# Performance work log

Hardware: AMD Instinct MI355X
Metric: run time of the kernel (lower is better)

The kernel has to match this reference:

```python
import jax, jax.numpy as jnp
import numpy as np

B, S, D, H = 2, 2048, 1024, 16
HD = D // H  # head dim = 64


def setup_inputs() -> dict:
    key = jax.random.key(0)
    ks = jax.random.split(key, 11)
    s = 0.02
    return {
        "query": jax.random.normal(ks[0], (B, S, D), jnp.float32),
        "key": jax.random.normal(ks[1], (B, S, D), jnp.float32),
        "value": jax.random.normal(ks[2], (B, S, D), jnp.float32),
        "Wq": jax.random.normal(ks[3], (D, D), jnp.float32) * s,
        "bq": jnp.zeros((D,), jnp.float32),
        "Wk": jax.random.normal(ks[4], (D, D), jnp.float32) * s,
        "bk": jnp.zeros((D,), jnp.float32),
        "Wv": jax.random.normal(ks[5], (D, D), jnp.float32) * s,
        "bv": jnp.zeros((D,), jnp.float32),
        "Wo": jax.random.normal(ks[6], (D, D), jnp.float32) * s,
        "bo": jnp.zeros((D,), jnp.float32),
    }


def reference(query, key, value, Wq, bq, Wk, bk, Wv, bv, Wo, bo):
    # Linear projections (torch Linear: x @ W^T + b; here W stored as [in, out])
    q = query @ Wq + bq  # [B,S,D]
    k = key @ Wk + bk
    v = value @ Wv + bv
    # split heads -> [B,H,S,HD]
    q = q.reshape(B, S, H, HD).transpose(0, 2, 1, 3)
    k = k.reshape(B, S, H, HD).transpose(0, 2, 1, 3)
    v = v.reshape(B, S, H, HD).transpose(0, 2, 1, 3)
    scores = jnp.einsum("bhqd,bhkd->bhqk", q, k) / jnp.sqrt(jnp.float32(HD))
    probs = jax.nn.softmax(scores, axis=-1)
    # dropout is identity at inference
    ctx = jnp.einsum("bhqk,bhkd->bhqd", probs, v)
    ctx = ctx.transpose(0, 2, 1, 3).reshape(B, S, D)
    return ctx @ Wo + bo
```

## Files before the change

kernel.cpp:

```cpp
#include <hip/hip_runtime.h>

#define BB 2
#define SS 2048
#define DD 1024
#define HH 16
#define HD 64
#define MM (BB*SS)

typedef __attribute__((ext_vector_type(8))) short bf16x8;
typedef __attribute__((ext_vector_type(4))) float f32x4;

static __device__ inline unsigned short f2bf(float x) {
    unsigned int u = __float_as_uint(x);
    unsigned int r = (u + 0x7fffu + ((u >> 16) & 1u)) >> 16;
    return (unsigned short)r;
}

static __device__ inline unsigned pack2bf(float lo, float hi) {
    return (unsigned)f2bf(lo) | ((unsigned)f2bf(hi) << 16);
}

static __device__ inline f32x4 mfma16(bf16x8 a, bf16x8 b, f32x4 c) {
    return __builtin_amdgcn_mfma_f32_16x16x32_bf16(a, b, c, 0, 0, 0);
}

static __device__ inline float fast_exp2(float x) {
    return __builtin_amdgcn_exp2f(x);
}

typedef __attribute__((address_space(3))) unsigned int lds_u32;
typedef const __attribute__((address_space(1))) unsigned int glb_u32;
static __device__ inline void async_ld16(const void* g, void* l) {
    __builtin_amdgcn_global_load_lds((glb_u32*)g, (lds_u32*)l, 16, 0, 0);
}

__global__ __launch_bounds__(256) void convert3_f32_bf16(const float* __restrict__ a,
                                                         const float* __restrict__ b,
                                                         const float* __restrict__ c,
                                                         unsigned short* __restrict__ oa,
                                                         unsigned short* __restrict__ ob,
                                                         unsigned short* __restrict__ oc,
                                                         int n) {
    const float* in = (blockIdx.z == 0) ? a : (blockIdx.z == 1) ? b : c;
    unsigned short* out = (blockIdx.z == 0) ? oa : (blockIdx.z == 1) ? ob : oc;
    int i = (blockIdx.x * 256 + threadIdx.x) * 4;
    if (i + 3 < n) {
        float4 v = *(const float4*)(in + i);
        ushort4 o;
        o.x = f2bf(v.x); o.y = f2bf(v.y); o.z = f2bf(v.z); o.w = f2bf(v.w);
        *(ushort4*)(out + i) = o;
    }
}

struct W4Args {
    const float* src[4];
    unsigned short* dst[4];
};
__global__ __launch_bounds__(256) void transpose4_f32_bf16(W4Args args) {
    __shared__ float tile[32][33];
    const float* in = args.src[blockIdx.z];
    unsigned short* out = args.dst[blockIdx.z];
    int c0 = blockIdx.x * 32, r0 = blockIdx.y * 32;
    int x = threadIdx.x;
    for (int yy = threadIdx.y; yy < 32; yy += 8)
        tile[yy][x] = in[(size_t)(r0 + yy) * DD + c0 + x];
    __syncthreads();
    for (int yy = threadIdx.y; yy < 32; yy += 8)
        out[(size_t)(c0 + yy) * DD + r0 + x] = f2bf(tile[x][yy]);
}

__global__ __launch_bounds__(256) void transpose_bf16_batched(const unsigned short* __restrict__ in,
                                                              unsigned short* __restrict__ out,
                                                              int R, int C) {
    __shared__ unsigned short tile[32][33];
    int z = blockIdx.z;
    const unsigned short* ib = in + (size_t)z * R * C;
    unsigned short* ob = out + (size_t)z * R * C;
    int c0 = blockIdx.x * 32, r0 = blockIdx.y * 32;
    int x = threadIdx.x;
    for (int yy = threadIdx.y; yy < 32; yy += 8)
        tile[yy][x] = ib[(size_t)(r0 + yy) * C + c0 + x];
    __syncthreads();
    for (int yy = threadIdx.y; yy < 32; yy += 8)
        ob[(size_t)(c0 + yy) * R + r0 + x] = tile[x][yy];
}

__device__ inline void cstore(float* C, size_t idx, float v) { C[idx] = v; }
__device__ inline void cstore(unsigned short* C, size_t idx, float v) { C[idx] = f2bf(v); }

template <typename OutT>
__device__ inline void gemm_bt_body(const unsigned short* __restrict__ A,
                                    const unsigned short* __restrict__ Bt,
                                    const float* __restrict__ bias,
                                    OutT* __restrict__ C,
                                    int M, int N, int K, float scale) {
    __shared__ alignas(16) unsigned short As[128 * 32];
    __shared__ alignas(16) unsigned short Bs[128 * 32];
    const int t = threadIdx.x;
    const int lane = t & 63, wave = t >> 6;
    const int quad = lane >> 4, l15 = lane & 15;
    const int wm = wave & 1, wn = wave >> 1;
    const int m0 = blockIdx.y * 128, n0 = blockIdx.x * 128;

    const unsigned short* gA = A + (size_t)(m0 + wave * 32 + (lane >> 2)) * K + (lane & 3) * 8;
    const unsigned short* gB = Bt + (size_t)(n0 + wave * 32 + (lane >> 2)) * K + (lane & 3) * 8;
    unsigned short* lA0 = &As[(wave * 32) * 32];
    unsigned short* lA1 = &As[(wave * 32 + 16) * 32];
    unsigned short* lB0 = &Bs[(wave * 32) * 32];
    unsigned short* lB1 = &Bs[(wave * 32 + 16) * 32];

    f32x4 acc[4][4];
#pragma unroll
    for (int i = 0; i < 4; i++)
#pragma unroll
        for (int j = 0; j < 4; j++) acc[i][j] = (f32x4){0.f, 0.f, 0.f, 0.f};

    for (int k0 = 0; k0 < K; k0 += 32) {
        __syncthreads();
        async_ld16(gA + k0, lA0);
        async_ld16(gA + (size_t)16 * K + k0, lA1);
        async_ld16(gB + k0, lB0);
        async_ld16(gB + (size_t)16 * K + k0, lB1);
        __syncthreads();

        bf16x8 af[4], bfr[4];
#pragma unroll
        for (int i = 0; i < 4; i++)
            af[i] = *(const bf16x8*)&As[(wm * 64 + i * 16 + l15) * 32 + quad * 8];
#pragma unroll
        for (int j = 0; j < 4; j++)
            bfr[j] = *(const bf16x8*)&Bs[(wn * 64 + j * 16 + l15) * 32 + quad * 8];
#pragma unroll
        for (int i = 0; i < 4; i++)
#pragma unroll
            for (int j = 0; j < 4; j++)
                acc[i][j] = mfma16(af[i], bfr[j], acc[i][j]);
    }

#pragma unroll
    for (int j = 0; j < 4; j++) {
        int col = n0 + wn * 64 + j * 16 + l15;
        float bv = bias[col];
#pragma unroll
        for (int i = 0; i < 4; i++) {
            int rowb = m0 + wm * 64 + i * 16 + quad * 4;
#pragma unroll
            for (int rr = 0; rr < 4; rr++) {
                float v = (acc[i][j][rr] + bv) * scale;
                cstore(C, (size_t)(rowb + rr) * N + col, v);
            }
        }
    }
}

struct QKVArgs {
    const unsigned short* A[3];
    const unsigned short* Bt[3];
    const float* bias[3];
    unsigned short* C[3];
};

#define QSCALE 0.1803368801111204f

__global__ __launch_bounds__(256) void gemm_qkv(QKVArgs args) {
    int z = blockIdx.z;
    float scale = (z == 0) ? QSCALE : 1.0f;
    gemm_bt_body<unsigned short>(args.A[z], args.Bt[z], args.bias[z], args.C[z],
                                 MM, DD, DD, scale);
}

__global__ __launch_bounds__(256) void gemm_out(const unsigned short* __restrict__ A,
                                                const unsigned short* __restrict__ Bt,
                                                const float* __restrict__ bias,
                                                float* __restrict__ C) {
    gemm_bt_body<float>(A, Bt, bias, C, MM, DD, DD, 1.0f);
}

#define TK 64
#define NTILE (SS / TK)
#define LDP 72

static __device__ inline void kv_step_lds(const unsigned short* __restrict__ Ksb,
                                          const unsigned short* __restrict__ Vsb,
                                          int kb0, bf16x8 qa0, bf16x8 qa1,
                                          f32x4 (&o)[4], float& lrow,
                                          int quad, int l15) {
    bf16x8 k0 = *(const bf16x8*)&Ksb[(kb0 + l15) * LDP + quad * 8];
    bf16x8 k1 = *(const bf16x8*)&Ksb[(kb0 + l15) * LDP + 32 + quad * 8];
    bf16x8 k2 = *(const bf16x8*)&Ksb[(kb0 + 16 + l15) * LDP + quad * 8];
    bf16x8 k3 = *(const bf16x8*)&Ksb[(kb0 + 16 + l15) * LDP + 32 + quad * 8];

    f32x4 sc0 = (f32x4){0.f, 0.f, 0.f, 0.f};
    f32x4 sc1 = (f32x4){0.f, 0.f, 0.f, 0.f};
    sc0 = mfma16(k0, qa0, sc0);
    sc0 = mfma16(k1, qa1, sc0);
    sc1 = mfma16(k2, qa0, sc1);
    sc1 = mfma16(k3, qa1, sc1);

    float p[8];
#pragma unroll
    for (int rr = 0; rr < 4; rr++) {
        p[rr]     = fast_exp2(sc0[rr]);
        p[rr + 4] = fast_exp2(sc1[rr]);
    }
    lrow += (p[0] + p[1]) + (p[2] + p[3]) + (p[4] + p[5]) + (p[6] + p[7]);

    union { unsigned u[4]; bf16x8 v; } pf;
    pf.u[0] = pack2bf(p[0], p[1]);
    pf.u[1] = pack2bf(p[2], p[3]);
    pf.u[2] = pack2bf(p[4], p[5]);
    pf.u[3] = pack2bf(p[6], p[7]);

#pragma unroll
    for (int j = 0; j < 4; j++) {
        union { ushort4 s[2]; bf16x8 v; } af;
        af.s[0] = *(const ushort4*)&Vsb[(j * 16 + l15) * LDP + kb0 + quad * 4];
        af.s[1] = *(const ushort4*)&Vsb[(j * 16 + l15) * LDP + kb0 + 16 + quad * 4];
        o[j] = mfma16(af.v, pf.v, o[j]);
    }
}

__global__ __launch_bounds__(256, 4) void flash_attn(const unsigned short* __restrict__ Q,
                                                     const unsigned short* __restrict__ Kg,
                                                     const unsigned short* __restrict__ Vt,
                                                     unsigned short* __restrict__ ctx) {
    __shared__ alignas(16) unsigned short Ks[2][TK * LDP];
    __shared__ alignas(16) unsigned short Vs[2][TK * LDP];
    const int t = threadIdx.x;
    const int lane = t & 63, wave = t >> 6;
    const int quad = lane >> 4, l15 = lane & 15;
    const int qg = blockIdx.x & 31;
    const int bh = blockIdx.x >> 5;
    const int h = bh & 15, b = bh >> 4;
    const int q0 = (qg * 4 + wave) * 16;

    const unsigned short* Qb = Q + (size_t)b * SS * DD + h * HD;
    const unsigned short* Kb = Kg + (size_t)b * SS * DD + h * HD;
    const unsigned short* Vb = Vt + ((size_t)b * DD + h * HD) * SS;

    const int r0 = t >> 3, cs = t & 7;
    const unsigned short* gK = Kb + (size_t)r0 * DD + cs * 8;
    const unsigned short* gV = Vb + (size_t)r0 * SS + cs * 8;
    const int ldsoff0 = r0 * LDP + cs * 8;
    const int ldsoff1 = (r0 + 32) * LDP + cs * 8;

    bf16x8 qa0 = *(const bf16x8*)(Qb + (size_t)(q0 + l15) * DD + quad * 8);
    bf16x8 qa1 = *(const bf16x8*)(Qb + (size_t)(q0 + l15) * DD + 32 + quad * 8);

    float lrow = 0.f;
    f32x4 o[4];
#pragma unroll
    for (int j = 0; j < 4; j++) o[j] = (f32x4){0.f, 0.f, 0.f, 0.f};

    {
        uint4 kr0 = *(const uint4*)(gK);
        uint4 kr1 = *(const uint4*)(gK + (size_t)32 * DD);
        uint4 vr0 = *(const uint4*)(gV);
        uint4 vr1 = *(const uint4*)(gV + (size_t)32 * SS);
        *(uint4*)&Ks[0][ldsoff0] = kr0;
        *(uint4*)&Ks[0][ldsoff1] = kr1;
        *(uint4*)&Vs[0][ldsoff0] = vr0;
        *(uint4*)&Vs[0][ldsoff1] = vr1;
    }
    __syncthreads();

    for (int tile = 0; tile < NTILE; ++tile) {
        const int buf = tile & 1;
        uint4 kr0, kr1, vr0, vr1;
        if (tile + 1 < NTILE) {
            const unsigned short* gKn = gK + (size_t)(tile + 1) * TK * DD;
            const unsigned short* gVn = gV + (tile + 1) * TK;
            kr0 = *(const uint4*)(gKn);
            kr1 = *(const uint4*)(gKn + (size_t)32 * DD);
            vr0 = *(const uint4*)(gVn);
            vr1 = *(const uint4*)(gVn + (size_t)32 * SS);
        }
        kv_step_lds(Ks[buf], Vs[buf], 0, qa0, qa1, o, lrow, quad, l15);
        kv_step_lds(Ks[buf], Vs[buf], 32, qa0, qa1, o, lrow, quad, l15);
        if (tile + 1 < NTILE) {
            __syncthreads();
            *(uint4*)&Ks[buf ^ 1][ldsoff0] = kr0;
            *(uint4*)&Ks[buf ^ 1][ldsoff1] = kr1;
            *(uint4*)&Vs[buf ^ 1][ldsoff0] = vr0;
            *(uint4*)&Vs[buf ^ 1][ldsoff1] = vr1;
            __syncthreads();
        }
    }

    lrow += __shfl_xor(lrow, 16, 64);
    lrow += __shfl_xor(lrow, 32, 64);
    float linv = 1.0f / lrow;

    unsigned short* crow = ctx + ((size_t)b * SS + q0 + l15) * DD + h * HD;
#pragma unroll
    for (int j = 0; j < 4; j++) {
        ushort4 w;
        w.x = f2bf(o[j][0] * linv); w.y = f2bf(o[j][1] * linv);
        w.z = f2bf(o[j][2] * linv); w.w = f2bf(o[j][3] * linv);
        *(ushort4*)(crow + j * 16 + quad * 4) = w;
    }
}

extern "C" void kernel_launch(void* const* d_in, const int* in_sizes, int n_in,
                              void* d_out, int out_size, void* d_ws, size_t ws_size,
                              hipStream_t stream) {
    const float* query = (const float*)d_in[0];
    const float* key   = (const float*)d_in[1];
    const float* value = (const float*)d_in[2];
    const float* Wq = (const float*)d_in[3];
    const float* bq = (const float*)d_in[4];
    const float* Wk = (const float*)d_in[5];
    const float* bk = (const float*)d_in[6];
    const float* Wv = (const float*)d_in[7];
    const float* bv = (const float*)d_in[8];
    const float* Wo = (const float*)d_in[9];
    const float* bo = (const float*)d_in[10];
    float* out = (float*)d_out;

    char* ws = (char*)d_ws;
    const size_t WSZ = (size_t)DD * DD * 2;
    const size_t XSZ = (size_t)MM * DD * 2;
    unsigned short* Wqt = (unsigned short*)(ws + 0 * WSZ);
    unsigned short* Wkt = (unsigned short*)(ws + 1 * WSZ);
    unsigned short* Wvt = (unsigned short*)(ws + 2 * WSZ);
    unsigned short* Wot = (unsigned short*)(ws + 3 * WSZ);
    unsigned short* Xq  = (unsigned short*)(ws + 4 * WSZ);
    unsigned short* Xk  = (unsigned short*)(ws + 4 * WSZ + 1 * XSZ);
    unsigned short* Xv  = (unsigned short*)(ws + 4 * WSZ + 2 * XSZ);
    unsigned short* Qp  = (unsigned short*)(ws + 4 * WSZ + 3 * XSZ);
    unsigned short* Kp  = (unsigned short*)(ws + 4 * WSZ + 4 * XSZ);
    unsigned short* Vp  = (unsigned short*)(ws + 4 * WSZ + 5 * XSZ);
    unsigned short* Vtp = Xq;
    unsigned short* ctx = Xk;

    const int n_act = MM * DD;

    convert3_f32_bf16<<<dim3(n_act / (256 * 4), 1, 3), 256, 0, stream>>>(
        query, key, value, Xq, Xk, Xv, n_act);

    W4Args wargs;
    wargs.src[0] = Wq; wargs.src[1] = Wk; wargs.src[2] = Wv; wargs.src[3] = Wo;
    wargs.dst[0] = Wqt; wargs.dst[1] = Wkt; wargs.dst[2] = Wvt; wargs.dst[3] = Wot;
    transpose4_f32_bf16<<<dim3(DD / 32, DD / 32, 4), dim3(32, 8), 0, stream>>>(wargs);

    QKVArgs args;
    args.A[0] = Xq; args.A[1] = Xk; args.A[2] = Xv;
    args.Bt[0] = Wqt; args.Bt[1] = Wkt; args.Bt[2] = Wvt;
    args.bias[0] = bq; args.bias[1] = bk; args.bias[2] = bv;
    args.C[0] = Qp; args.C[1] = Kp; args.C[2] = Vp;
    gemm_qkv<<<dim3(DD / 128, MM / 128, 3), 256, 0, stream>>>(args);

    transpose_bf16_batched<<<dim3(DD / 32, SS / 32, BB), dim3(32, 8), 0, stream>>>(Vp, Vtp, SS, DD);

    flash_attn<<<BB * HH * 32, 256, 0, stream>>>(Qp, Kp, Vtp, ctx);

    gemm_out<<<dim3(DD / 128, MM / 128), 256, 0, stream>>>(ctx, Wot, bo, out);
}
```

Measured before the change: 255.0 us.

## Merge prep kernels, fuse V transpose into QKV GEMM, double query rows per wave

```diff
diff --git a/kernel.cpp b/kernel.cpp
--- a/kernel.cpp
+++ b/kernel.cpp
@@ -34,55 +34,39 @@
     __builtin_amdgcn_global_load_lds((glb_u32*)g, (lds_u32*)l, 16, 0, 0);
 }
 
-__global__ __launch_bounds__(256) void convert3_f32_bf16(const float* __restrict__ a,
-                                                         const float* __restrict__ b,
-                                                         const float* __restrict__ c,
-                                                         unsigned short* __restrict__ oa,
-                                                         unsigned short* __restrict__ ob,
-                                                         unsigned short* __restrict__ oc,
-                                                         int n) {
-    const float* in = (blockIdx.z == 0) ? a : (blockIdx.z == 1) ? b : c;
-    unsigned short* out = (blockIdx.z == 0) ? oa : (blockIdx.z == 1) ? ob : oc;
-    int i = (blockIdx.x * 256 + threadIdx.x) * 4;
-    if (i + 3 < n) {
-        float4 v = *(const float4*)(in + i);
-        ushort4 o;
-        o.x = f2bf(v.x); o.y = f2bf(v.y); o.z = f2bf(v.z); o.w = f2bf(v.w);
-        *(ushort4*)(out + i) = o;
-    }
-}
-
-struct W4Args {
-    const float* src[4];
-    unsigned short* dst[4];
+struct PrepArgs {
+    const float* csrc[3];
+    unsigned short* cdst[3];
+    const float* wsrc[4];
+    unsigned short* wdst[4];
 };
-__global__ __launch_bounds__(256) void transpose4_f32_bf16(W4Args args) {
-    __shared__ float tile[32][33];
-    const float* in = args.src[blockIdx.z];
-    unsigned short* out = args.dst[blockIdx.z];
-    int c0 = blockIdx.x * 32, r0 = blockIdx.y * 32;
-    int x = threadIdx.x;
-    for (int yy = threadIdx.y; yy < 32; yy += 8)
-        tile[yy][x] = in[(size_t)(r0 + yy) * DD + c0 + x];
-    __syncthreads();
-    for (int yy = threadIdx.y; yy < 32; yy += 8)
-        out[(size_t)(c0 + yy) * DD + r0 + x] = f2bf(tile[x][yy]);
-}
-
-__global__ __launch_bounds__(256) void transpose_bf16_batched(const unsigned short* __restrict__ in,
-                                                              unsigned short* __restrict__ out,
-                                                              int R, int C) {
-    __shared__ unsigned short tile[32][33];
-    int z = blockIdx.z;
-    const unsigned short* ib = in + (size_t)z * R * C;
-    unsigned short* ob = out + (size_t)z * R * C;
-    int c0 = blockIdx.x * 32, r0 = blockIdx.y * 32;
-    int x = threadIdx.x;
-    for (int yy = threadIdx.y; yy < 32; yy += 8)
-        tile[yy][x] = ib[(size_t)(r0 + yy) * C + c0 + x];
-    __syncthreads();
-    for (int yy = threadIdx.y; yy < 32; yy += 8)
-        ob[(size_t)(c0 + yy) * R + r0 + x] = tile[x][yy];
+__global__ __launch_bounds__(256) void prep_inputs(PrepArgs args) {
+    const int z = blockIdx.z;
+    const int t = threadIdx.x;
+    if (z < 3) {
+        const float* in = args.csrc[z];
+        unsigned short* out = args.cdst[z];
+        int chunk = (blockIdx.y * 32 + blockIdx.x) * 4096;
+#pragma unroll
+        for (int r = 0; r < 4; r++) {
+            int i = chunk + r * 1024 + t * 4;
+            float4 v = *(const float4*)(in + i);
+            ushort4 o;
+            o.x = f2bf(v.x); o.y = f2bf(v.y); o.z = f2bf(v.z); o.w = f2bf(v.w);
+            *(ushort4*)(out + i) = o;
+        }
+    } else {
+        __shared__ float tile[32][33];
+        const float* in = args.wsrc[z - 3];
+        unsigned short* out = args.wdst[z - 3];
+        int c0 = blockIdx.x * 32, r0 = blockIdx.y * 32;
+        int x = t & 31, y0 = t >> 5;
+        for (int yy = y0; yy < 32; yy += 8)
+            tile[yy][x] = in[(size_t)(r0 + yy) * DD + c0 + x];
+        __syncthreads();
+        for (int yy = y0; yy < 32; yy += 8)
+            out[(size_t)(c0 + yy) * DD + r0 + x] = f2bf(tile[x][yy]);
+    }
 }
 
 __device__ inline void cstore(float* C, size_t idx, float v) { C[idx] = v; }
@@ -93,7 +77,7 @@
                                     const unsigned short* __restrict__ Bt,
                                     const float* __restrict__ bias,
                                     OutT* __restrict__ C,
-                                    int M, int N, int K, float scale) {
+                                    int M, int N, int K, float scale, int vt) {
     __shared__ alignas(16) unsigned short As[128 * 32];
     __shared__ alignas(16) unsigned short Bs[128 * 32];
     const int t = threadIdx.x;
@@ -137,17 +121,36 @@
                 acc[i][j] = mfma16(af[i], bfr[j], acc[i][j]);
     }
 
-#pragma unroll
-    for (int j = 0; j < 4; j++) {
-        int col = n0 + wn * 64 + j * 16 + l15;
-        float bv = bias[col];
-#pragma unroll
-        for (int i = 0; i < 4; i++) {
-            int rowb = m0 + wm * 64 + i * 16 + quad * 4;
-#pragma unroll
-            for (int rr = 0; rr < 4; rr++) {
-                float v = (acc[i][j][rr] + bv) * scale;
-                cstore(C, (size_t)(rowb + rr) * N + col, v);
+    if (vt) {
+#pragma unroll
+        for (int j = 0; j < 4; j++) {
+            int col = n0 + wn * 64 + j * 16 + l15;
+            float bv = bias[col];
+#pragma unroll
+            for (int i = 0; i < 4; i++) {
+                int rowb = m0 + wm * 64 + i * 16 + quad * 4;
+                int b = rowb >> 11, s = rowb & (SS - 1);
+                ushort4 w;
+                w.x = f2bf(acc[i][j][0] + bv);
+                w.y = f2bf(acc[i][j][1] + bv);
+                w.z = f2bf(acc[i][j][2] + bv);
+                w.w = f2bf(acc[i][j][3] + bv);
+                *(ushort4*)((unsigned short*)C + (size_t)b * DD * SS + (size_t)col * SS + s) = w;
+            }
+        }
+    } else {
+#pragma unroll
+        for (int j = 0; j < 4; j++) {
+            int col = n0 + wn * 64 + j * 16 + l15;
+            float bv = bias[col];
+#pragma unroll
+            for (int i = 0; i < 4; i++) {
+                int rowb = m0 + wm * 64 + i * 16 + quad * 4;
+#pragma unroll
+                for (int rr = 0; rr < 4; rr++) {
+                    float v = (acc[i][j][rr] + bv) * scale;
+                    cstore(C, (size_t)(rowb + rr) * N + col, v);
+                }
             }
         }
     }
@@ -166,61 +169,21 @@
     int z = blockIdx.z;
     float scale = (z == 0) ? QSCALE : 1.0f;
     gemm_bt_body<unsigned short>(args.A[z], args.Bt[z], args.bias[z], args.C[z],
-                                 MM, DD, DD, scale);
+                                 MM, DD, DD, scale, z == 2);
 }
 
 __global__ __launch_bounds__(256) void gemm_out(const unsigned short* __restrict__ A,
                                                 const unsigned short* __restrict__ Bt,
                                                 const float* __restrict__ bias,
                                                 float* __restrict__ C) {
-    gemm_bt_body<float>(A, Bt, bias, C, MM, DD, DD, 1.0f);
+    gemm_bt_body<float>(A, Bt, bias, C, MM, DD, DD, 1.0f, 0);
 }
 
 #define TK 64
 #define NTILE (SS / TK)
 #define LDP 72
 
-static __device__ inline void kv_step_lds(const unsigned short* __restrict__ Ksb,
-                                          const unsigned short* __restrict__ Vsb,
-                                          int kb0, bf16x8 qa0, bf16x8 qa1,
-                                          f32x4 (&o)[4], float& lrow,
-                                          int quad, int l15) {
-    bf16x8 k0 = *(const bf16x8*)&Ksb[(kb0 + l15) * LDP + quad * 8];
-    bf16x8 k1 = *(const bf16x8*)&Ksb[(kb0 + l15) * LDP + 32 + quad * 8];
-    bf16x8 k2 = *(const bf16x8*)&Ksb[(kb0 + 16 + l15) * LDP + quad * 8];
-    bf16x8 k3 = *(const bf16x8*)&Ksb[(kb0 + 16 + l15) * LDP + 32 + quad * 8];
-
-    f32x4 sc0 = (f32x4){0.f, 0.f, 0.f, 0.f};
-    f32x4 sc1 = (f32x4){0.f, 0.f, 0.f, 0.f};
-    sc0 = mfma16(k0, qa0, sc0);
-    sc0 = mfma16(k1, qa1, sc0);
-    sc1 = mfma16(k2, qa0, sc1);
-    sc1 = mfma16(k3, qa1, sc1);
-
-    float p[8];
-#pragma unroll
-    for (int rr = 0; rr < 4; rr++) {
-        p[rr]     = fast_exp2(sc0[rr]);
-        p[rr + 4] = fast_exp2(sc1[rr]);
-    }
-    lrow += (p[0] + p[1]) + (p[2] + p[3]) + (p[4] + p[5]) + (p[6] + p[7]);
-
-    union { unsigned u[4]; bf16x8 v; } pf;
-    pf.u[0] = pack2bf(p[0], p[1]);
-    pf.u[1] = pack2bf(p[2], p[3]);
-    pf.u[2] = pack2bf(p[4], p[5]);
-    pf.u[3] = pack2bf(p[6], p[7]);
-
-#pragma unroll
-    for (int j = 0; j < 4; j++) {
-        union { ushort4 s[2]; bf16x8 v; } af;
-        af.s[0] = *(const ushort4*)&Vsb[(j * 16 + l15) * LDP + kb0 + quad * 4];
-        af.s[1] = *(const ushort4*)&Vsb[(j * 16 + l15) * LDP + kb0 + 16 + quad * 4];
-        o[j] = mfma16(af.v, pf.v, o[j]);
-    }
-}
-
-__global__ __launch_bounds__(256, 4) void flash_attn(const unsigned short* __restrict__ Q,
+__global__ __launch_bounds__(256, 2) void flash_attn(const unsigned short* __restrict__ Q,
                                                      const unsigned short* __restrict__ Kg,
                                                      const unsigned short* __restrict__ Vt,
                                                      unsigned short* __restrict__ ctx) {
@@ -229,10 +192,10 @@
     const int t = threadIdx.x;
     const int lane = t & 63, wave = t >> 6;
     const int quad = lane >> 4, l15 = lane & 15;
-    const int qg = blockIdx.x & 31;
-    const int bh = blockIdx.x >> 5;
+    const int qg = blockIdx.x & 15;
+    const int bh = blockIdx.x >> 4;
     const int h = bh & 15, b = bh >> 4;
-    const int q0 = (qg * 4 + wave) * 16;
+    const int q0 = (qg * 4 + wave) * 32;
 
     const unsigned short* Qb = Q + (size_t)b * SS * DD + h * HD;
     const unsigned short* Kb = Kg + (size_t)b * SS * DD + h * HD;
@@ -244,13 +207,19 @@
     const int ldsoff0 = r0 * LDP + cs * 8;
     const int ldsoff1 = (r0 + 32) * LDP + cs * 8;
 
-    bf16x8 qa0 = *(const bf16x8*)(Qb + (size_t)(q0 + l15) * DD + quad * 8);
-    bf16x8 qa1 = *(const bf16x8*)(Qb + (size_t)(q0 + l15) * DD + 32 + quad * 8);
-
-    float lrow = 0.f;
-    f32x4 o[4];
-#pragma unroll
-    for (int j = 0; j < 4; j++) o[j] = (f32x4){0.f, 0.f, 0.f, 0.f};
+    bf16x8 qa[2][2];
+#pragma unroll
+    for (int qt = 0; qt < 2; qt++) {
+        qa[qt][0] = *(const bf16x8*)(Qb + (size_t)(q0 + qt * 16 + l15) * DD + quad * 8);
+        qa[qt][1] = *(const bf16x8*)(Qb + (size_t)(q0 + qt * 16 + l15) * DD + 32 + quad * 8);
+    }
+
+    float lrow[2] = {0.f, 0.f};
+    f32x4 o[2][4];
+#pragma unroll
+    for (int qt = 0; qt < 2; qt++)
+#pragma unroll
+        for (int j = 0; j < 4; j++) o[qt][j] = (f32x4){0.f, 0.f, 0.f, 0.f};
 
     {
         uint4 kr0 = *(const uint4*)(gK);
@@ -275,8 +244,49 @@
             vr0 = *(const uint4*)(gVn);
             vr1 = *(const uint4*)(gVn + (size_t)32 * SS);
         }
-        kv_step_lds(Ks[buf], Vs[buf], 0, qa0, qa1, o, lrow, quad, l15);
-        kv_step_lds(Ks[buf], Vs[buf], 32, qa0, qa1, o, lrow, quad, l15);
+        const unsigned short* Ksb = Ks[buf];
+        const unsigned short* Vsb = Vs[buf];
+#pragma unroll
+        for (int half = 0; half < 2; half++) {
+            const int kb0 = half * 32;
+            bf16x8 k0 = *(const bf16x8*)&Ksb[(kb0 + l15) * LDP + quad * 8];
+            bf16x8 k1 = *(const bf16x8*)&Ksb[(kb0 + l15) * LDP + 32 + quad * 8];
+            bf16x8 k2 = *(const bf16x8*)&Ksb[(kb0 + 16 + l15) * LDP + quad * 8];
+            bf16x8 k3 = *(const bf16x8*)&Ksb[(kb0 + 16 + l15) * LDP + 32 + quad * 8];
+            union { ushort4 s[2]; bf16x8 v; } af[4];
+#pragma unroll
+            for (int j = 0; j < 4; j++) {
+                af[j].s[0] = *(const ushort4*)&Vsb[(j * 16 + l15) * LDP + kb0 + quad * 4];
+                af[j].s[1] = *(const ushort4*)&Vsb[(j * 16 + l15) * LDP + kb0 + 16 + quad * 4];
+            }
+#pragma unroll
+            for (int qt = 0; qt < 2; qt++) {
+                f32x4 sc0 = (f32x4){0.f, 0.f, 0.f, 0.f};
+                f32x4 sc1 = (f32x4){0.f, 0.f, 0.f, 0.f};
+                sc0 = mfma16(k0, qa[qt][0], sc0);
+                sc0 = mfma16(k1, qa[qt][1], sc0);
+                sc1 = mfma16(k2, qa[qt][0], sc1);
+                sc1 = mfma16(k3, qa[qt][1], sc1);
+
+                float p[8];
+#pragma unroll
+                for (int rr = 0; rr < 4; rr++) {
+                    p[rr]     = fast_exp2(sc0[rr]);
+                    p[rr + 4] = fast_exp2(sc1[rr]);
+                }
+                lrow[qt] += (p[0] + p[1]) + (p[2] + p[3]) + (p[4] + p[5]) + (p[6] + p[7]);
+
+                union { unsigned u[4]; bf16x8 v; } pf;
+                pf.u[0] = pack2bf(p[0], p[1]);
+                pf.u[1] = pack2bf(p[2], p[3]);
+                pf.u[2] = pack2bf(p[4], p[5]);
+                pf.u[3] = pack2bf(p[6], p[7]);
+
+#pragma unroll
+                for (int j = 0; j < 4; j++)
+                    o[qt][j] = mfma16(af[j].v, pf.v, o[qt][j]);
+            }
+        }
         if (tile + 1 < NTILE) {
             __syncthreads();
             *(uint4*)&Ks[buf ^ 1][ldsoff0] = kr0;
@@ -287,17 +297,20 @@
         }
     }
 
-    lrow += __shfl_xor(lrow, 16, 64);
-    lrow += __shfl_xor(lrow, 32, 64);
-    float linv = 1.0f / lrow;
-
-    unsigned short* crow = ctx + ((size_t)b * SS + q0 + l15) * DD + h * HD;
-#pragma unroll
-    for (int j = 0; j < 4; j++) {
-        ushort4 w;
-        w.x = f2bf(o[j][0] * linv); w.y = f2bf(o[j][1] * linv);
-        w.z = f2bf(o[j][2] * linv); w.w = f2bf(o[j][3] * linv);
-        *(ushort4*)(crow + j * 16 + quad * 4) = w;
+#pragma unroll
+    for (int qt = 0; qt < 2; qt++) {
+        float l = lrow[qt];
+        l += __shfl_xor(l, 16, 64);
+        l += __shfl_xor(l, 32, 64);
+        float linv = 1.0f / l;
+        unsigned short* crow = ctx + ((size_t)b * SS + q0 + qt * 16 + l15) * DD + h * HD;
+#pragma unroll
+        for (int j = 0; j < 4; j++) {
+            ushort4 w;
+            w.x = f2bf(o[qt][j][0] * linv); w.y = f2bf(o[qt][j][1] * linv);
+            w.z = f2bf(o[qt][j][2] * linv); w.w = f2bf(o[qt][j][3] * linv);
+            *(ushort4*)(crow + j * 16 + quad * 4) = w;
+        }
     }
 }
 
@@ -329,30 +342,24 @@
     unsigned short* Xv  = (unsigned short*)(ws + 4 * WSZ + 2 * XSZ);
     unsigned short* Qp  = (unsigned short*)(ws + 4 * WSZ + 3 * XSZ);
     unsigned short* Kp  = (unsigned short*)(ws + 4 * WSZ + 4 * XSZ);
-    unsigned short* Vp  = (unsigned short*)(ws + 4 * WSZ + 5 * XSZ);
-    unsigned short* Vtp = Xq;
+    unsigned short* Vtp = (unsigned short*)(ws + 4 * WSZ + 5 * XSZ);
     unsigned short* ctx = Xk;
 
-    const int n_act = MM * DD;
-
-    convert3_f32_bf16<<<dim3(n_act / (256 * 4), 1, 3), 256, 0, stream>>>(
-        query, key, value, Xq, Xk, Xv, n_act);
-
-    W4Args wargs;
-    wargs.src[0] = Wq; wargs.src[1] = Wk; wargs.src[2] = Wv; wargs.src[3] = Wo;
-    wargs.dst[0] = Wqt; wargs.dst[1] = Wkt; wargs.dst[2] = Wvt; wargs.dst[3] = Wot;
-    transpose4_f32_bf16<<<dim3(DD / 32, DD / 32, 4), dim3(32, 8), 0, stream>>>(wargs);
+    PrepArgs pargs;
+    pargs.csrc[0] = query; pargs.csrc[1] = key; pargs.csrc[2] = value;
+    pargs.cdst[0] = Xq; pargs.cdst[1] = Xk; pargs.cdst[2] = Xv;
+    pargs.wsrc[0] = Wq; pargs.wsrc[1] = Wk; pargs.wsrc[2] = Wv; pargs.wsrc[3] = Wo;
+    pargs.wdst[0] = Wqt; pargs.wdst[1] = Wkt; pargs.wdst[2] = Wvt; pargs.wdst[3] = Wot;
+    prep_inputs<<<dim3(32, 32, 7), 256, 0, stream>>>(pargs);
 
     QKVArgs args;
     args.A[0] = Xq; args.A[1] = Xk; args.A[2] = Xv;
     args.Bt[0] = Wqt; args.Bt[1] = Wkt; args.Bt[2] = Wvt;
     args.bias[0] = bq; args.bias[1] = bk; args.bias[2] = bv;
-    args.C[0] = Qp; args.C[1] = Kp; args.C[2] = Vp;
+    args.C[0] = Qp; args.C[1] = Kp; args.C[2] = Vtp;
     gemm_qkv<<<dim3(DD / 128, MM / 128, 3), 256, 0, stream>>>(args);
 
-    transpose_bf16_batched<<<dim3(DD / 32, SS / 32, BB), dim3(32, 8), 0, stream>>>(Vp, Vtp, SS, DD);
-
-    flash_attn<<<BB * HH * 32, 256, 0, stream>>>(Qp, Kp, Vtp, ctx);
+    flash_attn<<<BB * HH * 16, 256, 0, stream>>>(Qp, Kp, Vtp, ctx);
 
     gemm_out<<<dim3(DD / 128, MM / 128), 256, 0, stream>>>(ctx, Wot, bo, out);
 }
```

After: 251.0 us. Within noise of the previous version (-1.6%).
